# Performance work log

Hardware: AMD Instinct MI355X
Metric: run time of the kernel (lower is better)

Reference implementation:

```python
import jax, jax.numpy as jnp
import numpy as np

H = 32          # num_heads
D = 64          # kv_channels (head dim)
HID = 2048      # hidden_size
MAXPOS = 2048   # max_seq_length


def _rotary_table(num_pos, dim):
    # [num_pos, dim]: sin for first dim/2 cols, cos for last dim/2 cols
    inv_freq = 1.0 / (10000.0 ** (jnp.arange(0, dim, 2, dtype=jnp.float32) / dim))
    t = jnp.arange(num_pos, dtype=jnp.float32)[:, None] * inv_freq[None, :]
    return jnp.concatenate([jnp.sin(t), jnp.cos(t)], axis=1)


def _apply_rope(x, sin, cos):
    # x: [B,S,H,D]; sin,cos: [B,S,D/2]
    sin = jnp.concatenate([sin, sin], axis=-1)[:, :, None, :]  # [B,S,1,D]
    cos = jnp.concatenate([cos, cos], axis=-1)[:, :, None, :]
    half = x.shape[-1] // 2
    x1, x2 = x[..., :half], x[..., half:]
    rot = jnp.concatenate([-x2, x1], axis=-1)
    return x * cos + rot * sin


def setup_inputs() -> dict:
    key = jax.random.key(0)
    k1, k2, k3, k4 = jax.random.split(key, 4)
    B, S = 2, 2048
    hidden_states = jax.random.normal(k1, (B, S, HID), jnp.float32)
    attention_mask = jax.random.randint(k2, (B, 1, S, S), 0, 2).astype(bool)
    position_ids = jnp.broadcast_to(jnp.arange(S, dtype=jnp.int32)[None, :], (B, S))
    W_qkv = jax.random.normal(k3, (3 * H * D, HID), jnp.float32) * 0.02
    W_o = jax.random.normal(k4, (HID, H * D), jnp.float32) * 0.02
    return {"hidden_states": hidden_states, "attention_mask": attention_mask,
            "position_ids": position_ids, "W_qkv": W_qkv, "W_o": W_o}


def reference(hidden_states, attention_mask, position_ids, W_qkv, W_o):
    B, S, _ = hidden_states.shape
    # fused QKV projection (nn.Linear: x @ W.T, no bias)
    qkv = hidden_states @ W_qkv.T                       # [B,S,3*H*D]
    qkv = qkv.reshape(B, S, H, 3 * D)
    q, k, v = jnp.split(qkv, 3, axis=-1)                # each [B,S,H,D]
    sincos = _rotary_table(MAXPOS, D)[position_ids]     # [B,S,D]
    sin, cos = jnp.split(sincos, 2, axis=-1)            # [B,S,D/2] each
    q = _apply_rope(q, sin, cos)
    k = _apply_rope(k, sin, cos)
    scale = jnp.sqrt(jnp.float32(D))
    scores = jnp.einsum('bqhd,bkhd->bhqk', q, k) / scale   # [B,H,S,S]
    scores = jnp.where(attention_mask, jnp.float32(-10000.0), scores)
    weights = jax.nn.softmax(scores, axis=-1)
    attn = jnp.einsum('bhqk,bkhd->bqhd', weights, v)       # [B,S,H,D]
    attn = attn.reshape(B, S, H * D)
    return attn @ W_o.T                                    # [B,S,HID]
```

## Files before the change

kernel.cpp:

```cpp
#include <hip/hip_runtime.h>

#define B_   2
#define S_   2048
#define H_   32
#define D_   64
#define HID_ 2048

typedef unsigned short ushort_t;
typedef __attribute__((ext_vector_type(8))) short short8;
typedef __attribute__((ext_vector_type(4))) float floatx4;

typedef const __attribute__((address_space(1))) char* gas_ptr;
typedef __attribute__((address_space(3))) char* las_ptr;

__device__ __forceinline__ float bf2f(ushort_t u) {
    union { unsigned int i; float f; } v; v.i = ((unsigned int)u) << 16; return v.f;
}
__device__ __forceinline__ ushort_t f2bf(float f) {
    union { float f; unsigned int i; } v; v.f = f;
    unsigned int x = v.i;
    unsigned int r = x + 0x7fffu + ((x >> 16) & 1u);
    return (ushort_t)(r >> 16);
}

__device__ __forceinline__ float fexp2(float x) {
#if __has_builtin(__builtin_amdgcn_exp2f)
    return __builtin_amdgcn_exp2f(x);
#else
    float r; asm("v_exp_f32 %0, %1" : "=v"(r) : "v"(x)); return r;
#endif
}

__device__ __forceinline__ unsigned cvt_pk_bf16(float a, float b) {
    unsigned r;
    asm("v_cvt_pk_bf16_f32 %0, %1, %2" : "=v"(r) : "v"(a), "v"(b));
    return r;
}

__global__ __launch_bounds__(256) void cast_f32_bf16(const float* __restrict__ in,
                                                     ushort_t* __restrict__ out,
                                                     int n8) {
    int i = blockIdx.x * 256 + threadIdx.x;
    if (i >= n8) return;
    const float4* p = (const float4*)(in + (size_t)i * 8);
    float4 a = p[0], b = p[1];
    uint4 o;
    o.x = cvt_pk_bf16(a.x, a.y);
    o.y = cvt_pk_bf16(a.z, a.w);
    o.z = cvt_pk_bf16(b.x, b.y);
    o.w = cvt_pk_bf16(b.z, b.w);
    *(uint4*)(out + (size_t)i * 8) = o;
}

__global__ __launch_bounds__(256) void mask_pack(const int* __restrict__ m,
                                                 unsigned long long* __restrict__ bits) {
    int idx = blockIdx.x * 256 + threadIdx.x;
    unsigned long long bal = __ballot(m[idx] != 0);
    if ((threadIdx.x & 63) == 0) bits[idx >> 6] = bal;
}

__global__ __launch_bounds__(512, 2) void gemm256_bt(const ushort_t* __restrict__ A,
                                                     const ushort_t* __restrict__ Bm,
                                                     ushort_t* __restrict__ C,
                                                     int M, int N, int K) {
    __shared__ ushort_t lA[2][256][64];
    __shared__ ushort_t lB[2][256][64];
    const int tid  = threadIdx.x;
    const int w    = tid >> 6, lane = tid & 63;
    const int quad = lane >> 4, l16 = lane & 15;
    const int wm = w >> 2, wn = w & 3;
    const int sr = lane >> 3, ss = lane & 7;
    const int gseg = (ss ^ sr) * 8;

    const int nbx = N >> 8;
    int id  = blockIdx.x;
    int cpx = gridDim.x >> 3;
    int swz = (id & 7) * cpx + (id >> 3);
    int by = swz / nbx, bx = swz - by * nbx;
    const int m0 = by * 256, n0 = bx * 256;

    int arow[2], brow[2];
    arow[0] = w * 8;                       arow[1] = 128 + w * 8;
    brow[0] = (w >> 2) * 64 + (w & 3) * 8; brow[1] = 128 + brow[0];

    const ushort_t *gAf[2], *gAs[2], *gBf[2], *gBs[2];
#pragma unroll
    for (int c = 0; c < 2; c++) {
        gAf[c] = A  + (size_t)(m0 + arow[c] + sr) * K + gseg;
        gAs[c] = A  + (size_t)(m0 + arow[c] + 64 + sr) * K + gseg;
        gBf[c] = Bm + (size_t)(n0 + brow[c] + sr) * K + gseg;
        gBs[c] = Bm + (size_t)(n0 + brow[c] + 32 + sr) * K + gseg;
    }

#define STAGE_AF(BUF, KT) do { _Pragma("unroll") for (int c = 0; c < 2; c++) \
    __builtin_amdgcn_global_load_lds((gas_ptr)(gAf[c] + (KT)), (las_ptr)&lA[BUF][arow[c]][0], 16, 0, 0); } while (0)
#define STAGE_AS(BUF, KT) do { _Pragma("unroll") for (int c = 0; c < 2; c++) \
    __builtin_amdgcn_global_load_lds((gas_ptr)(gAs[c] + (KT)), (las_ptr)&lA[BUF][arow[c] + 64][0], 16, 0, 0); } while (0)
#define STAGE_BF(BUF, KT) do { _Pragma("unroll") for (int c = 0; c < 2; c++) \
    __builtin_amdgcn_global_load_lds((gas_ptr)(gBf[c] + (KT)), (las_ptr)&lB[BUF][brow[c]][0], 16, 0, 0); } while (0)
#define STAGE_BS(BUF, KT) do { _Pragma("unroll") for (int c = 0; c < 2; c++) \
    __builtin_amdgcn_global_load_lds((gas_ptr)(gBs[c] + (KT)), (las_ptr)&lB[BUF][brow[c] + 32][0], 16, 0, 0); } while (0)

#define LDA_(Hh, BUF) do { _Pragma("unroll") for (int mi = 0; mi < 4; mi++) \
    _Pragma("unroll") for (int ks = 0; ks < 2; ks++) \
        aF[mi][ks] = *(const short8*)&lA[BUF][wm * 128 + (Hh) * 64 + mi * 16 + l16][(((ks * 4 + quad) ^ (l16 & 7)) * 8)]; } while (0)
#define LDB_(Gg, BUF) do { _Pragma("unroll") for (int ni = 0; ni < 2; ni++) \
    _Pragma("unroll") for (int ks = 0; ks < 2; ks++) \
        bF[Gg][ni][ks] = *(const short8*)&lB[BUF][wn * 64 + (Gg) * 32 + ni * 16 + l16][(((ks * 4 + quad) ^ (l16 & 7)) * 8)]; } while (0)

#define MM_(Hh, Gg) do { _Pragma("unroll") for (int mi = 0; mi < 4; mi++) \
    _Pragma("unroll") for (int ni = 0; ni < 2; ni++) \
    _Pragma("unroll") for (int ks = 0; ks < 2; ks++) \
        acc[(Hh) * 4 + mi][(Gg) * 2 + ni] = __builtin_amdgcn_mfma_f32_16x16x32_bf16( \
            aF[mi][ks], bF[Gg][ni][ks], acc[(Hh) * 4 + mi][(Gg) * 2 + ni], 0, 0, 0); } while (0)

    floatx4 acc[8][4];
#pragma unroll
    for (int i = 0; i < 8; i++)
#pragma unroll
        for (int j = 0; j < 4; j++) acc[i][j] = (floatx4){0.f, 0.f, 0.f, 0.f};
    short8 aF[4][2];
    short8 bF[2][2][2];

    const int NT = K >> 6;

    STAGE_AF(0, 0); STAGE_BF(0, 0); STAGE_BS(0, 0); STAGE_AS(0, 0);
    STAGE_AF(1, 64); STAGE_BF(1, 64); STAGE_BS(1, 64);
    asm volatile("s_waitcnt vmcnt(6)" ::: "memory");
    __builtin_amdgcn_s_barrier();

    for (int t = 0; t < NT; ++t) {
        const int buf = t & 1, nb = buf ^ 1;
        const int kt1 = (t + 1) << 6, kt2 = (t + 2) << 6;
        const bool g1 = (t + 1 < NT), g2 = (t + 2 < NT);

        LDA_(0, buf); LDB_(0, buf);
        if (g1) STAGE_AS(nb, kt1);
        __builtin_amdgcn_s_barrier();
        __builtin_amdgcn_s_setprio(1);
        MM_(0, 0);
        __builtin_amdgcn_s_setprio(0);
        __builtin_amdgcn_s_barrier();

        LDB_(1, buf);
        if (g2) STAGE_AF(buf, kt2);
        __builtin_amdgcn_s_barrier();
        __builtin_amdgcn_s_setprio(1);
        MM_(0, 1);
        __builtin_amdgcn_s_setprio(0);
        __builtin_amdgcn_s_barrier();

        LDA_(1, buf);
        if (g2) STAGE_BF(buf, kt2);
        __builtin_amdgcn_s_barrier();
        __builtin_amdgcn_s_setprio(1);
        MM_(1, 1);
        __builtin_amdgcn_s_setprio(0);
        __builtin_amdgcn_s_barrier();

        if (g2) STAGE_BS(buf, kt2);
        __builtin_amdgcn_s_barrier();
        __builtin_amdgcn_s_setprio(1);
        MM_(1, 0);
        __builtin_amdgcn_s_setprio(0);

        if (t < NT - 2)       { asm volatile("s_waitcnt vmcnt(6)" ::: "memory"); }
        else if (t == NT - 2) { asm volatile("s_waitcnt vmcnt(0)" ::: "memory"); }
        __builtin_amdgcn_s_barrier();
    }

#pragma unroll
    for (int mi = 0; mi < 8; mi++)
#pragma unroll
        for (int ni = 0; ni < 4; ni++)
#pragma unroll
            for (int r = 0; r < 4; r++) {
                int row = m0 + wm * 128 + mi * 16 + quad * 4 + r;
                int col = n0 + wn * 64 + ni * 16 + l16;
                C[(size_t)row * N + col] = f2bf(acc[mi][ni][r]);
            }
#undef STAGE_AF
#undef STAGE_AS
#undef STAGE_BF
#undef STAGE_BS
#undef LDA_
#undef LDB_
#undef MM_
}

template <bool OF32>
__global__ __launch_bounds__(256) void gemm_bt(const ushort_t* __restrict__ A,
                                               const ushort_t* __restrict__ Bm,
                                               void* __restrict__ Cv,
                                               int M, int N, int K) {
    __shared__ ushort_t lA[128 * 32];
    __shared__ ushort_t lB[128 * 32];
    const int tid  = threadIdx.x;
    const int lane = tid & 63, wave = tid >> 6;
    const int quad = lane >> 4, l16 = lane & 15;
    const int wm = wave >> 1, wn = wave & 1;
    const int m0 = blockIdx.y * 128, n0 = blockIdx.x * 128;

    const int srow = tid >> 2;
    const int gseg = (tid & 3) ^ ((tid >> 3) & 3);
    const ushort_t* gA = A + (size_t)(m0 + srow) * K + gseg * 8;
    const ushort_t* gB = Bm + (size_t)(n0 + srow) * K + gseg * 8;

    const int fseg = quad ^ ((l16 >> 1) & 3);

    floatx4 acc[4][4];
#pragma unroll
    for (int i = 0; i < 4; i++)
#pragma unroll
        for (int j = 0; j < 4; j++) acc[i][j] = (floatx4){0.f, 0.f, 0.f, 0.f};

    for (int k0 = 0; k0 < K; k0 += 32) {
#pragma unroll
        for (int j = 0; j < 2; j++) {
            __builtin_amdgcn_global_load_lds(
                (gas_ptr)(gA + (size_t)j * 64 * K + k0),
                (las_ptr)(lA + j * 2048 + wave * 512), 16, 0, 0);
            __builtin_amdgcn_global_load_lds(
                (gas_ptr)(gB + (size_t)j * 64 * K + k0),
                (las_ptr)(lB + j * 2048 + wave * 512), 16, 0, 0);
        }
        __syncthreads();

        short8 aF[4], bF[4];
#pragma unroll
        for (int mi = 0; mi < 4; mi++)
            aF[mi] = *(const short8*)&lA[(wm * 64 + mi * 16 + l16) * 32 + fseg * 8];
#pragma unroll
        for (int ni = 0; ni < 4; ni++)
            bF[ni] = *(const short8*)&lB[(wn * 64 + ni * 16 + l16) * 32 + fseg * 8];
#pragma unroll
        for (int mi = 0; mi < 4; mi++)
#pragma unroll
            for (int ni = 0; ni < 4; ni++)
                acc[mi][ni] = __builtin_amdgcn_mfma_f32_16x16x32_bf16(aF[mi], bF[ni], acc[mi][ni], 0, 0, 0);
        __syncthreads();
    }

#pragma unroll
    for (int mi = 0; mi < 4; mi++)
#pragma unroll
        for (int ni = 0; ni < 4; ni++)
#pragma unroll
            for (int r = 0; r < 4; r++) {
                int row = m0 + wm * 64 + mi * 16 + quad * 4 + r;
                int col = n0 + wn * 64 + ni * 16 + l16;
                if (OF32) ((float*)Cv)[(size_t)row * N + col] = acc[mi][ni][r];
                else      ((ushort_t*)Cv)[(size_t)row * N + col] = f2bf(acc[mi][ni][r]);
            }
}

__global__ __launch_bounds__(256) void rope_qk(const ushort_t* __restrict__ qkv,
                                               const int* __restrict__ pos,
                                               ushort_t* __restrict__ qr,
                                               ushort_t* __restrict__ kr) {
    int idx = blockIdx.x * 256 + threadIdx.x;
    int d = idx & 63;
    int s = (idx >> 6) & 2047;
    int h = (idx >> 17) & 31;
    int b = idx >> 22;
    size_t qbase = ((size_t)(b * S_ + s)) * (3 * H_ * D_) + h * (3 * D_);
    int i  = d & 31;
    int d2 = d ^ 32;
    float x   = bf2f(qkv[qbase + d]);
    float xp  = bf2f(qkv[qbase + d2]);
    float kx  = bf2f(qkv[qbase + 64 + d]);
    float kxp = bf2f(qkv[qbase + 64 + d2]);
    int   p   = pos[b * S_ + s];
    float inv = fexp2((float)i * -0.41524101186092985f);
    float t   = (float)p * inv;
    float c = cosf(t), sn = sinf(t);
    float rq = (d < 32) ? -xp : xp;
    float rk = (d < 32) ? -kxp : kxp;
    float qo = (x * c + rq * sn) * 0.18033688011112042f;
    float ko = kx * c + rk * sn;
    size_t o = ((size_t)(b * H_ + h) * S_ + s) * D_ + d;
    qr[o] = f2bf(qo);
    kr[o] = f2bf(ko);
}

__global__ __launch_bounds__(256) void v_trans(const ushort_t* __restrict__ qkv,
                                               ushort_t* __restrict__ vt) {
    __shared__ ushort_t tile[64][72];
    const int bid = blockIdx.x;
    const int g  = bid >> 5;
    const int s0 = (bid & 31) * 64;
    const int b = g >> 5, h = g & 31;
    const int tid = threadIdx.x;
    const int r = tid >> 2, c = (tid & 3) * 16;
    const ushort_t* src = qkv + ((size_t)(b * S_) + s0 + r) * (3 * H_ * D_) + h * (3 * D_) + 128 + c;
    *(short8*)&tile[r][c]     = *(const short8*)src;
    *(short8*)&tile[r][c + 8] = *(const short8*)(src + 8);
    __syncthreads();
    const int d = tid >> 2, cs = (tid & 3) * 16;
    ushort_t* dst = vt + ((size_t)g * D_ + d) * S_ + s0 + cs;
    short8 o0, o1;
#pragma unroll
    for (int j = 0; j < 8; j++) {
        o0[j] = (short)tile[cs + j][d];
        o1[j] = (short)tile[cs + 8 + j][d];
    }
    *(short8*)dst       = o0;
    *(short8*)(dst + 8) = o1;
}

__global__ __launch_bounds__(256) void attn_kernel(const ushort_t* __restrict__ qr,
                                                   const ushort_t* __restrict__ kr,
                                                   const ushort_t* __restrict__ vt,
                                                   const unsigned long long* __restrict__ mbits,
                                                   ushort_t* __restrict__ ctx) {
    __shared__ ushort_t lK[64 * 64];
    __shared__ ushort_t lV[64 * 64];
    __shared__ ushort_t lds_p[4][16][72];
    const int tid  = threadIdx.x;
    const int wave = tid >> 6, lane = tid & 63;
    const int quad = lane >> 4, l16 = lane & 15;

    const int id   = blockIdx.x;
    const int g    = (id & 7) | ((id >> 8) << 3);
    const int qblk = (id >> 3) & 31;
    const int b    = g >> 5;
    const int q0   = qblk * 64 + wave * 16;
    const size_t headBase = (size_t)g * S_ * D_;
    const unsigned long long* mrow = mbits + ((size_t)b * S_ + q0 + l16) * (S_ / 64);

    const int sr = lane >> 3, ss = lane & 7;
    const int gss = ss ^ sr;
    const ushort_t* gK0 = kr + headBase + (size_t)(wave * 16 + sr) * D_ + gss * 8;
    const ushort_t* gV0 = vt + headBase + (size_t)(wave * 16 + sr) * S_ + gss * 8;

    const int segA0 = ((quad)     ^ (l16 & 7)) * 8;
    const int segA1 = ((quad + 4) ^ (l16 & 7)) * 8;
    const int rowOff = (l16)*64;

    short8 qf0 = *(const short8*)(qr + headBase + (size_t)(q0 + l16) * D_ + quad * 8);
    short8 qf1 = *(const short8*)(qr + headBase + (size_t)(q0 + l16) * D_ + 32 + quad * 8);

    float l_st = 0.f;
    floatx4 o[4];
#pragma unroll
    for (int t = 0; t < 4; t++) o[t] = (floatx4){0.f, 0.f, 0.f, 0.f};

    for (int k0 = 0; k0 < S_; k0 += 64) {
#pragma unroll
        for (int i = 0; i < 2; i++) {
            __builtin_amdgcn_global_load_lds(
                (gas_ptr)(gK0 + (size_t)(k0 + i * 8) * D_),
                (las_ptr)(lK + (wave * 16 + i * 8) * 64), 16, 0, 0);
            __builtin_amdgcn_global_load_lds(
                (gas_ptr)(gV0 + (size_t)(i * 8) * S_ + k0),
                (las_ptr)(lV + (wave * 16 + i * 8) * 64), 16, 0, 0);
        }
        unsigned long long mb = mrow[k0 >> 6];
        __syncthreads();

        floatx4 scT[4];
#pragma unroll
        for (int t = 0; t < 4; t++) scT[t] = (floatx4){0.f, 0.f, 0.f, 0.f};
#pragma unroll
        for (int t = 0; t < 4; t++) {
            short8 kf0 = *(const short8*)&lK[t * 1024 + rowOff + segA0];
            short8 kf1 = *(const short8*)&lK[t * 1024 + rowOff + segA1];
            scT[t] = __builtin_amdgcn_mfma_f32_16x16x32_bf16(kf0, qf0, scT[t], 0, 0, 0);
            scT[t] = __builtin_amdgcn_mfma_f32_16x16x32_bf16(kf1, qf1, scT[t], 0, 0, 0);
        }

        unsigned mlo = (unsigned)(mb >> (quad * 4));
        unsigned mhi = (unsigned)(mb >> (quad * 4 + 32));
        float pv[4][4];
        float rs = 0.f;
#pragma unroll
        for (int t = 0; t < 4; t++) {
            unsigned msrc = (t < 2) ? mlo : mhi;
#pragma unroll
            for (int r = 0; r < 4; r++) {
                int bitpos = (t & 1) * 16 + r;
                float e = fexp2(scT[t][r]);
                e = ((msrc >> bitpos) & 1u) ? 0.f : e;
                pv[t][r] = e;
                rs += e;
            }
        }
        l_st += rs;

#pragma unroll
        for (int t = 0; t < 4; t++) {
            uint2 w;
            w.x = cvt_pk_bf16(pv[t][0], pv[t][1]);
            w.y = cvt_pk_bf16(pv[t][2], pv[t][3]);
            *(uint2*)&lds_p[wave][l16][t * 16 + quad * 4] = w;
        }
        short8 pf0 = *(const short8*)&lds_p[wave][l16][quad * 8];
        short8 pf1 = *(const short8*)&lds_p[wave][l16][32 + quad * 8];

#pragma unroll
        for (int t = 0; t < 4; t++) {
            short8 vf0 = *(const short8*)&lV[t * 1024 + rowOff + segA0];
            short8 vf1 = *(const short8*)&lV[t * 1024 + rowOff + segA1];
            o[t] = __builtin_amdgcn_mfma_f32_16x16x32_bf16(pf0, vf0, o[t], 0, 0, 0);
            o[t] = __builtin_amdgcn_mfma_f32_16x16x32_bf16(pf1, vf1, o[t], 0, 0, 0);
        }
        __syncthreads();
    }

    l_st += __shfl_xor(l_st, 16);
    l_st += __shfl_xor(l_st, 32);
    float li[4];
#pragma unroll
    for (int r = 0; r < 4; r++) li[r] = 1.0f / __shfl(l_st, quad * 4 + r, 16);
#pragma unroll
    for (int t = 0; t < 4; t++)
#pragma unroll
        for (int r = 0; r < 4; r++) {
            int srow = q0 + quad * 4 + r;
            ctx[((size_t)(b * S_) + srow) * (H_ * D_) + (g & 31) * D_ + t * 16 + l16] = f2bf(o[t][r] * li[r]);
        }
}

extern "C" void kernel_launch(void* const* d_in, const int* in_sizes, int n_in,
                              void* d_out, int out_size, void* d_ws, size_t ws_size,
                              hipStream_t stream) {
    const float* hidden          = (const float*)d_in[0];
    const int* mask              = (const int*)d_in[1];
    const int* pos               = (const int*)d_in[2];
    const float* Wqkv            = (const float*)d_in[3];
    const float* Wo              = (const float*)d_in[4];
    float* out                   = (float*)d_out;

    char* ws = (char*)d_ws;
    ushort_t* qkv     = (ushort_t*)(ws);
    ushort_t* ctx     = (ushort_t*)(ws);
    unsigned long long* mbits = (unsigned long long*)(ws + 16777216);
    ushort_t* Wo_bf   = (ushort_t*)(ws + 50331648);
    ushort_t* hid_bf  = (ushort_t*)(ws + 58720256);
    ushort_t* Wqkv_bf = (ushort_t*)(ws + 75497472);
    ushort_t* q_r     = (ushort_t*)(ws + 58720256);
    ushort_t* k_r     = (ushort_t*)(ws + 75497472);
    ushort_t* v_t     = (ushort_t*)(ws + 92274688);

    {
        int n8 = (B_ * S_ * HID_) / 8;
        cast_f32_bf16<<<n8 / 256, 256, 0, stream>>>(hidden, hid_bf, n8);
        n8 = (3 * H_ * D_ * HID_) / 8;
        cast_f32_bf16<<<n8 / 256, 256, 0, stream>>>(Wqkv, Wqkv_bf, n8);
        n8 = (HID_ * H_ * D_) / 8;
        cast_f32_bf16<<<n8 / 256, 256, 0, stream>>>(Wo, Wo_bf, n8);
    }

    gemm256_bt<<<((3 * H_ * D_) / 256) * ((B_ * S_) / 256), 512, 0, stream>>>(
        hid_bf, Wqkv_bf, qkv, B_ * S_, 3 * H_ * D_, HID_);

    int nElem = B_ * H_ * S_ * D_;
    rope_qk<<<nElem / 256, 256, 0, stream>>>(qkv, pos, q_r, k_r);
    v_trans<<<B_ * H_ * (S_ / 64), 256, 0, stream>>>(qkv, v_t);

    mask_pack<<<(B_ * S_ * S_) / 256, 256, 0, stream>>>(mask, mbits);

    attn_kernel<<<2048, 256, 0, stream>>>(q_r, k_r, v_t, mbits, ctx);

    gemm_bt<true><<<dim3(HID_ / 128, (B_ * S_) / 128), 256, 0, stream>>>(
        ctx, Wo_bf, out, B_ * S_, HID_, H_ * D_);
}
```

Baseline: 358.1 us.

## Restructure GEMM main loop into two-tile unrolled pipeline with reordered staging

After: 363.2 us. Within noise of the previous version (+1.4%).

```diff
diff --git a/kernel.cpp b/kernel.cpp
--- a/kernel.cpp
+++ b/kernel.cpp
@@ -101,18 +101,23 @@
 #define STAGE_BS(BUF, KT) do { _Pragma("unroll") for (int c = 0; c < 2; c++) \
     __builtin_amdgcn_global_load_lds((gas_ptr)(gBs[c] + (KT)), (las_ptr)&lB[BUF][brow[c] + 32][0], 16, 0, 0); } while (0)
 
-#define LDA_(Hh, BUF) do { _Pragma("unroll") for (int mi = 0; mi < 4; mi++) \
+#define LDA_(SUB, BUF) do { _Pragma("unroll") for (int mi = 0; mi < 4; mi++) \
     _Pragma("unroll") for (int ks = 0; ks < 2; ks++) \
-        aF[mi][ks] = *(const short8*)&lA[BUF][wm * 128 + (Hh) * 64 + mi * 16 + l16][(((ks * 4 + quad) ^ (l16 & 7)) * 8)]; } while (0)
-#define LDB_(Gg, BUF) do { _Pragma("unroll") for (int ni = 0; ni < 2; ni++) \
+        aF[mi][ks] = *(const short8*)&lA[BUF][wm * 128 + (SUB) * 64 + mi * 16 + l16][(((ks * 4 + quad) ^ (l16 & 7)) * 8)]; } while (0)
+#define LDB_(SUB, BUF) do { _Pragma("unroll") for (int ni = 0; ni < 2; ni++) \
     _Pragma("unroll") for (int ks = 0; ks < 2; ks++) \
-        bF[Gg][ni][ks] = *(const short8*)&lB[BUF][wn * 64 + (Gg) * 32 + ni * 16 + l16][(((ks * 4 + quad) ^ (l16 & 7)) * 8)]; } while (0)
+        bF[ni][ks] = *(const short8*)&lB[BUF][wn * 64 + (SUB) * 32 + ni * 16 + l16][(((ks * 4 + quad) ^ (l16 & 7)) * 8)]; } while (0)
 
 #define MM_(Hh, Gg) do { _Pragma("unroll") for (int mi = 0; mi < 4; mi++) \
     _Pragma("unroll") for (int ni = 0; ni < 2; ni++) \
     _Pragma("unroll") for (int ks = 0; ks < 2; ks++) \
         acc[(Hh) * 4 + mi][(Gg) * 2 + ni] = __builtin_amdgcn_mfma_f32_16x16x32_bf16( \
-            aF[mi][ks], bF[Gg][ni][ks], acc[(Hh) * 4 + mi][(Gg) * 2 + ni], 0, 0, 0); } while (0)
+            aF[mi][ks], bF[ni][ks], acc[(Hh) * 4 + mi][(Gg) * 2 + ni], 0, 0, 0); } while (0)
+
+#define VMC6 asm volatile("s_waitcnt vmcnt(6)" ::: "memory")
+#define BARR __builtin_amdgcn_s_barrier()
+#define SETP1 __builtin_amdgcn_s_setprio(1)
+#define SETP0 __builtin_amdgcn_s_setprio(0)
 
     floatx4 acc[8][4];
 #pragma unroll
@@ -120,53 +125,60 @@
 #pragma unroll
         for (int j = 0; j < 4; j++) acc[i][j] = (floatx4){0.f, 0.f, 0.f, 0.f};
     short8 aF[4][2];
-    short8 bF[2][2][2];
+    short8 bF[2][2];
 
     const int NT = K >> 6;
-
-    STAGE_AF(0, 0); STAGE_BF(0, 0); STAGE_BS(0, 0); STAGE_AS(0, 0);
-    STAGE_AF(1, 64); STAGE_BF(1, 64); STAGE_BS(1, 64);
-    asm volatile("s_waitcnt vmcnt(6)" ::: "memory");
-    __builtin_amdgcn_s_barrier();
-
-    for (int t = 0; t < NT; ++t) {
-        const int buf = t & 1, nb = buf ^ 1;
-        const int kt1 = (t + 1) << 6, kt2 = (t + 2) << 6;
-        const bool g1 = (t + 1 < NT), g2 = (t + 2 < NT);
-
-        LDA_(0, buf); LDB_(0, buf);
-        if (g1) STAGE_AS(nb, kt1);
-        __builtin_amdgcn_s_barrier();
-        __builtin_amdgcn_s_setprio(1);
-        MM_(0, 0);
-        __builtin_amdgcn_s_setprio(0);
-        __builtin_amdgcn_s_barrier();
-
-        LDB_(1, buf);
-        if (g2) STAGE_AF(buf, kt2);
-        __builtin_amdgcn_s_barrier();
-        __builtin_amdgcn_s_setprio(1);
-        MM_(0, 1);
-        __builtin_amdgcn_s_setprio(0);
-        __builtin_amdgcn_s_barrier();
-
-        LDA_(1, buf);
-        if (g2) STAGE_BF(buf, kt2);
-        __builtin_amdgcn_s_barrier();
-        __builtin_amdgcn_s_setprio(1);
-        MM_(1, 1);
-        __builtin_amdgcn_s_setprio(0);
-        __builtin_amdgcn_s_barrier();
-
-        if (g2) STAGE_BS(buf, kt2);
-        __builtin_amdgcn_s_barrier();
-        __builtin_amdgcn_s_setprio(1);
-        MM_(1, 0);
-        __builtin_amdgcn_s_setprio(0);
-
-        if (t < NT - 2)       { asm volatile("s_waitcnt vmcnt(6)" ::: "memory"); }
-        else if (t == NT - 2) { asm volatile("s_waitcnt vmcnt(0)" ::: "memory"); }
-        __builtin_amdgcn_s_barrier();
+    const int NI = NT >> 1;
+
+    STAGE_AF(0, 0); STAGE_BF(0, 0); STAGE_AS(0, 0); STAGE_BS(0, 0);
+    STAGE_BF(1, 64); STAGE_AS(1, 64); STAGE_BS(1, 64);
+    VMC6;
+    BARR;
+
+    for (int i = 0; i < NI; ++i) {
+        const int t0k = i << 7;
+        const int t1k = t0k + 64;
+        const int t2k = t0k + 128, t3k = t0k + 192;
+        const bool g2 = (t2k < K), g3 = (t3k < K);
+        const bool last = (i == NI - 1);
+
+        LDA_(0, 0); LDB_(0, 0);
+        STAGE_AF(1, t1k);
+        asm volatile("s_waitcnt lgkmcnt(8)" ::: "memory");
+        BARR; SETP1; MM_(0, 0); SETP0;
+        VMC6; BARR;
+        LDA_(1, 0);
+        if (g2) STAGE_BF(0, t2k);
+        BARR; SETP1; MM_(1, 0); SETP0;
+        VMC6; BARR;
+        LDB_(1, 0);
+        if (g2) STAGE_AS(0, t2k);
+        BARR; SETP1; MM_(1, 1); SETP0;
+        VMC6; BARR;
+        LDA_(0, 0);
+        if (g2) STAGE_BS(0, t2k);
+        BARR; SETP1; MM_(0, 1); SETP0;
+        if (last) { asm volatile("s_waitcnt vmcnt(0)" ::: "memory"); }
+        else      { VMC6; }
+        BARR;
+
+        LDA_(0, 1); LDB_(0, 1);
+        if (g2) STAGE_AF(0, t2k);
+        asm volatile("s_waitcnt lgkmcnt(8)" ::: "memory");
+        BARR; SETP1; MM_(0, 0); SETP0;
+        VMC6; BARR;
+        LDA_(1, 1);
+        if (g3) STAGE_BF(1, t3k);
+        BARR; SETP1; MM_(1, 0); SETP0;
+        VMC6; BARR;
+        LDB_(1, 1);
+        if (g3) STAGE_AS(1, t3k);
+        BARR; SETP1; MM_(1, 1); SETP0;
+        VMC6; BARR;
+        LDA_(0, 1);
+        if (g3) STAGE_BS(1, t3k);
+        BARR; SETP1; MM_(0, 1); SETP0;
+        VMC6; BARR;
     }
 
 #pragma unroll
@@ -186,6 +198,10 @@
 #undef LDA_
 #undef LDB_
 #undef MM_
+#undef VMC6
+#undef BARR
+#undef SETP1
+#undef SETP0
 }
 
 template <bool OF32>
```
